# Kernel optimization log

Measured on AMD Instinct MI355X. Metric: run time of the kernel, lower is better.

Reference implementation:

```python
import jax, jax.numpy as jnp
import numpy as np

TOP_K = 2
CAPACITY_FACTOR = 1.0


def setup_inputs() -> dict:
    key = jax.random.key(0)
    ks = jax.random.split(key, 4)
    S, M, E, V = 32768, 512, 64, 2048
    return {
        "x": jax.random.normal(ks[0], (S, M), jnp.float32),
        "wg": jax.random.normal(ks[1], (E, M), jnp.float32) * (1.0 / np.sqrt(M)),
        "fc1_w": jax.random.normal(ks[2], (E, M, V), jnp.float32) * (1.0 / np.sqrt(M)),
        "fc1_b": jnp.zeros((E, V), jnp.float32),
        "fc2_w": jax.random.normal(ks[3], (E, V, M), jnp.float32) * (1.0 / np.sqrt(V)),
        "fc2_b": jnp.zeros((E, M), jnp.float32),
    }


def _moe_forward(x, wg, fc1_w, fc1_b, fc2_w, fc2_b):
    S, M = x.shape
    E = wg.shape[0]
    K = TOP_K
    # capacity = top_k * int(cap_factor * ceil(S / E))  (static, from shapes)
    C = K * int(CAPACITY_FACTOR * ((S + E - 1) // E))

    # --- gating ---
    logits = x @ wg.T                                    # [S, E]
    gates = jax.nn.softmax(logits, axis=-1)              # [S, E]
    topk_idx = jax.lax.top_k(logits, K)[1]               # [S, K] int32
    masks = jax.nn.one_hot(topk_idx, E, dtype=logits.dtype)  # [S, K, E]
    gates_s = jnp.einsum('se,ske->sk', gates, masks)     # [S, K]

    # load-balance aux loss (fp32 path of load_balance)
    me = gates.sum(axis=0)                               # [E]
    ce = masks[:, 0, :].sum(axis=0)                      # [E]
    l_loss = jnp.sum(me * ce) * (E / (S * S))

    # --- cumsum capacity locations with per-k offsets (acc_base) ---
    counts = masks.sum(axis=0)                           # [K, E]
    prev_counts = jnp.concatenate(
        [jnp.zeros((1, E), logits.dtype), jnp.cumsum(counts, axis=0)[:-1]], axis=0)
    cums = jnp.cumsum(masks, axis=0) - 1.0               # fast_cumsum_sub_one per k
    locs = jnp.einsum('ske,ske->sk', cums + prev_counts[None], masks).astype(jnp.int32)

    # normalize top-k gates (top_k > 1 branch)
    denom = jnp.maximum(gates_s.sum(axis=1, keepdims=True),
                        jnp.finfo(gates_s.dtype).eps)
    gates_n = gates_s / denom                            # [S, K]

    # --- encode: scatter tokens into [E, C, M], overflow tokens dropped ---
    valid = locs < C                                     # [S, K]
    flat_pos = jnp.where(valid, topk_idx.astype(jnp.int32) * C + locs, E * C)
    src = jnp.broadcast_to(x[:, None, :], (S, K, M)).reshape(-1, M)
    disp = jnp.zeros((E * C + 1, M), x.dtype).at[flat_pos.reshape(-1)].add(src)
    disp = disp[:E * C].reshape(E, C, M)                 # world_size=1: AllToAll = id

    # --- fused FFN experts: relu(x @ fc1 + b1) @ fc2 + b2 ---
    h = jax.nn.relu(jnp.einsum('ecm,emv->ecv', disp, fc1_w) + fc1_b[:, None, :])
    eout = jnp.einsum('ecv,evm->ecm', h, fc2_w) + fc2_b[:, None, :]

    # --- decode/combine: gather expert slots, weight by normalized gates ---
    eflat = jnp.concatenate([eout.reshape(E * C, M),
                             jnp.zeros((1, M), eout.dtype)], axis=0)
    gathered = eflat[flat_pos]                           # [S, K, M]
    y = jnp.einsum('sk,skm->sm', gates_n * valid.astype(gates_n.dtype), gathered)
    return y, l_loss


def reference(x, wg, fc1_w, fc1_b, fc2_w, fc2_b):
    return _moe_forward(x, wg, fc1_w, fc1_b, fc2_w, fc2_b)
```

## Files before the change

kernel.cpp:

```cpp
#include <hip/hip_runtime.h>
#include <hip/hip_bf16.h>
#include <stdint.h>

#define S_TOK 32768
#define M_DIM 512
#define E_NUM 64
#define V_DIM 2048
#define CAP   1024

typedef __attribute__((ext_vector_type(8))) short short8;
typedef __attribute__((ext_vector_type(4))) float f32x4;

__device__ __forceinline__ unsigned short f2bf(float f) {
  unsigned int u = __float_as_uint(f);
  unsigned int r = (u + 0x7fffu + ((u >> 16) & 1u)) >> 16;
  return (unsigned short)r;
}
__device__ __forceinline__ float bf2f(unsigned short h) {
  return __uint_as_float(((unsigned int)h) << 16);
}

__device__ __forceinline__ void gload16(const void* g, void* lds) {
  __builtin_amdgcn_global_load_lds(
      (const __attribute__((address_space(1))) void*)g,
      (__attribute__((address_space(3))) void*)lds, 16, 0, 0);
}

__global__ __launch_bounds__(256) void transpose_convert(const float* __restrict__ in,
                                                         unsigned short* __restrict__ out,
                                                         int R, int Cc) {
  __shared__ float tile[32][33];
  int b = blockIdx.z;
  const float* ip = in + (size_t)b * R * Cc;
  unsigned short* op = out + (size_t)b * R * Cc;
  int c0 = blockIdx.x * 32, r0 = blockIdx.y * 32;
  int tx = threadIdx.x & 31, ty = threadIdx.x >> 5;
  #pragma unroll
  for (int j = 0; j < 32; j += 8)
    tile[ty + j][tx] = ip[(size_t)(r0 + ty + j) * Cc + c0 + tx];
  __syncthreads();
  int tid = threadIdx.x;
  #pragma unroll
  for (int j = 0; j < 32; j += 16) {
    int c = (tid >> 4) + j;
    int r2 = (tid & 15) * 2;
    ushort2 o;
    o.x = f2bf(tile[r2][c]);
    o.y = f2bf(tile[r2 + 1][c]);
    *reinterpret_cast<ushort2*>(&op[(size_t)(c0 + c) * R + r0 + r2]) = o;
  }
}

__global__ __launch_bounds__(256) void gating_kernel(
    const float* __restrict__ x, const float* __restrict__ wg,
    int* __restrict__ topk, float* __restrict__ gates_n,
    float* __restrict__ me_part, int* __restrict__ ce_part,
    unsigned short* __restrict__ xbf) {
  __shared__ float4 xs4[16 * 128];
  __shared__ float mered[4][64];
  __shared__ int cered[4][64];
  int tid = threadIdx.x;
  int l = tid & 63, w = tid >> 6;
  int tb = blockIdx.x * 16;
  const float4* xg4 = reinterpret_cast<const float4*>(x) + (size_t)tb * 128;
  ushort4* xb4 = reinterpret_cast<ushort4*>(xbf) + (size_t)tb * 128;
  #pragma unroll
  for (int i = 0; i < 8; ++i) {
    float4 v = xg4[i * 256 + tid];
    xs4[i * 256 + tid] = v;
    ushort4 o;
    o.x = f2bf(v.x); o.y = f2bf(v.y); o.z = f2bf(v.z); o.w = f2bf(v.w);
    xb4[i * 256 + tid] = o;
  }
  __syncthreads();

  const float4* wg4 = reinterpret_cast<const float4*>(wg) + (size_t)l * 128;
  float acc[4] = {0.f, 0.f, 0.f, 0.f};
  for (int i = 0; i < 128; ++i) {
    float4 wv = wg4[i];
    #pragma unroll
    for (int t = 0; t < 4; ++t) {
      float4 xv = xs4[(w * 4 + t) * 128 + i];
      acc[t] += xv.x * wv.x; acc[t] += xv.y * wv.y;
      acc[t] += xv.z * wv.z; acc[t] += xv.w * wv.w;
    }
  }

  float melocal = 0.f;
  int celocal = 0;
  for (int t = 0; t < 4; ++t) {
    float v = acc[t];
    float bv = v; int bi = l;
    #pragma unroll
    for (int off = 32; off; off >>= 1) {
      float ov = __shfl_xor(bv, off);
      int oi = __shfl_xor(bi, off);
      if (ov > bv || (ov == bv && oi < bi)) { bv = ov; bi = oi; }
    }
    float v2 = (l == bi) ? -INFINITY : v;
    float bv2 = v2; int bi2 = l;
    #pragma unroll
    for (int off = 32; off; off >>= 1) {
      float ov = __shfl_xor(bv2, off);
      int oi = __shfl_xor(bi2, off);
      if (ov > bv2 || (ov == bv2 && oi < bi2)) { bv2 = ov; bi2 = oi; }
    }
    float ex = expf(v - bv);
    float s = ex;
    #pragma unroll
    for (int off = 32; off; off >>= 1) s += __shfl_xor(s, off);
    melocal += ex / s;
    if (l == bi) celocal += 1;
    if (l == 0) {
      int sidx = tb + w * 4 + t;
      topk[sidx * 2 + 0] = bi;
      topk[sidx * 2 + 1] = bi2;
      float g1 = 1.0f / s;
      float g2 = expf(bv2 - bv) / s;
      float denom = fmaxf(g1 + g2, 1.1920929e-07f);
      gates_n[sidx * 2 + 0] = g1 / denom;
      gates_n[sidx * 2 + 1] = g2 / denom;
    }
  }
  mered[w][l] = melocal;
  cered[w][l] = celocal;
  __syncthreads();
  if (tid < 64) {
    me_part[blockIdx.x * 64 + tid] =
        mered[0][tid] + mered[1][tid] + mered[2][tid] + mered[3][tid];
    ce_part[blockIdx.x * 64 + tid] =
        cered[0][tid] + cered[1][tid] + cered[2][tid] + cered[3][tid];
  }
}

__global__ __launch_bounds__(256) void rank_kernel(const int* __restrict__ topk,
                                                   int* __restrict__ dest,
                                                   int* __restrict__ slot_map) {
  int e = blockIdx.x;
  int tid = threadIdx.x;
  int l = tid & 63, w = tid >> 6;
  const int2* tk = reinterpret_cast<const int2*>(topk);
  int base = tid * 128;
  int c0 = 0, c1 = 0;
  for (int j = 0; j < 128; ++j) {
    int2 p = tk[base + j];
    c0 += (p.x == e); c1 += (p.y == e);
  }
  int i0 = c0, i1 = c1;
  #pragma unroll
  for (int off = 1; off < 64; off <<= 1) {
    int t0 = __shfl_up(i0, off);
    int t1 = __shfl_up(i1, off);
    if (l >= off) { i0 += t0; i1 += t1; }
  }
  __shared__ int ws0[4], ws1[4], wo0[4], wo1[4], tot0s;
  if (l == 63) { ws0[w] = i0; ws1[w] = i1; }
  __syncthreads();
  if (tid == 0) {
    int a = 0, b = 0;
    #pragma unroll
    for (int j = 0; j < 4; ++j) { wo0[j] = a; a += ws0[j]; wo1[j] = b; b += ws1[j]; }
    tot0s = a;
  }
  __syncthreads();
  int loc0 = wo0[w] + i0 - c0;
  int loc1 = tot0s + wo1[w] + i1 - c1;
  for (int j = 0; j < 128; ++j) {
    int s = base + j;
    int2 p = tk[s];
    if (p.x == e) {
      int d = (loc0 < CAP) ? e * CAP + loc0 : -1;
      dest[s * 2] = d;
      if (d >= 0) slot_map[d] = s;
      loc0++;
    }
    if (p.y == e) {
      int d = (loc1 < CAP) ? e * CAP + loc1 : -1;
      dest[s * 2 + 1] = d;
      if (d >= 0) slot_map[d] = s;
      loc1++;
    }
  }
}

#define PH_TOP                                                                 \
  __builtin_amdgcn_sched_barrier(0);                                           \
  __builtin_amdgcn_s_barrier();                                                \
  asm volatile("s_waitcnt lgkmcnt(0)" ::: "memory");                           \
  __builtin_amdgcn_sched_barrier(0);                                           \
  __builtin_amdgcn_s_setprio(1);
#define PH_BOT                                                                 \
  __builtin_amdgcn_s_setprio(0);                                               \
  __builtin_amdgcn_sched_barrier(0);                                           \
  __builtin_amdgcn_s_barrier();

struct SmemGemm {
  union {
    struct {
      unsigned short A[2][256 * 64];
      unsigned short B[2][256 * 64];
    } st;
    unsigned short C[256 * 258];
  };
};

template <int KD, int ND, int NBX, int NBY, bool GATHER, bool RELU>
__global__ __launch_bounds__(512, 2) void gemm8_kernel(
    const unsigned short* __restrict__ A,
    const unsigned short* __restrict__ BT,
    const float* __restrict__ bias,
    const int* __restrict__ slot_map,
    unsigned short* __restrict__ out) {
  constexpr int NT = KD / 64;
  __shared__ SmemGemm sm;

  const int tid = threadIdx.x;
  const int l = tid & 63;
  const int w = tid >> 6;
  const int wm = w >> 2;
  const int wn = w & 3;
  const int lr = l & 15;
  const int lk8 = l >> 4;

  const int nwg = E_NUM * NBX * NBY;
  const int cpx = nwg >> 3;
  int lid = ((int)blockIdx.x % 8) * cpx + (int)blockIdx.x / 8;
  const int e = lid / (NBX * NBY);
  int rem = lid % (NBX * NBY);
  const int n0 = (rem / NBY) * 256;
  const int r0 = (rem % NBY) * 256;

  const int cg8 = (((l & 7) ^ (l >> 3)) * 8);

  uint32_t offA[2][2], offB[2][2], ldsA[2][2], ldsB[2][2];
  #pragma unroll
  for (int sel = 0; sel < 2; ++sel) {
    #pragma unroll
    for (int i = 0; i < 2; ++i) {
      int lr128 = i * 64 + w * 8 + (l >> 3);
      int ar = ((lr128 >> 6) * 128) + sel * 64 + (lr128 & 63);
      int br = ((lr128 >> 5) * 64) + sel * 32 + (lr128 & 31);
      ldsA[sel][i] = ar * 64 + (l & 7) * 8;
      ldsB[sel][i] = br * 64 + (l & 7) * 8;
      int arow;
      if (GATHER) {
        int s = slot_map[e * CAP + r0 + ar];
        if (s < 0) s = 0;
        arow = s;
      } else {
        arow = e * CAP + r0 + ar;
      }
      offA[sel][i] = (uint32_t)arow * KD + cg8;
      offB[sel][i] = (uint32_t)(n0 + br) * KD + cg8;
    }
  }
  const unsigned short* Bexp = BT + (size_t)e * ND * KD;

#define STAGE_A(sel, p, kt)                                                    \
  do {                                                                         \
    gload16(A + offA[sel][0] + (kt) * 64, &sm.st.A[p][ldsA[sel][0]]);          \
    gload16(A + offA[sel][1] + (kt) * 64, &sm.st.A[p][ldsA[sel][1]]);          \
  } while (0)
#define STAGE_B(sel, p, kt)                                                    \
  do {                                                                         \
    gload16(Bexp + offB[sel][0] + (kt) * 64, &sm.st.B[p][ldsB[sel][0]]);       \
    gload16(Bexp + offB[sel][1] + (kt) * 64, &sm.st.B[p][ldsB[sel][1]]);       \
  } while (0)

  const int sg0 = ((0 + lk8) ^ (lr & 7)) * 8;
  const int sg1 = ((4 + lk8) ^ (lr & 7)) * 8;
#define RD_A(p, mh, mi, ks)                                                    \
  (*reinterpret_cast<const short8*>(                                           \
      &sm.st.A[p][(wm * 128 + (mh) * 64 + (mi) * 16 + lr) * 64 + ((ks) ? sg1 : sg0)]))
#define RD_B(p, nh, ni, ks)                                                    \
  (*reinterpret_cast<const short8*>(                                           \
      &sm.st.B[p][(wn * 64 + (nh) * 32 + (ni) * 16 + lr) * 64 + ((ks) ? sg1 : sg0)]))

  short8 afr[2][4][2];
  short8 bfr[2][2];
  f32x4 acc[8][4];
  f32x4 zero = {0.f, 0.f, 0.f, 0.f};
  #pragma unroll
  for (int m = 0; m < 8; ++m)
    #pragma unroll
    for (int n = 0; n < 4; ++n) acc[m][n] = zero;

  STAGE_A(0, 0, 0); STAGE_A(1, 0, 0); STAGE_B(0, 0, 0); STAGE_B(1, 0, 0);
  STAGE_A(0, 1, 1); STAGE_A(1, 1, 1); STAGE_B(0, 1, 1);
  asm volatile("s_waitcnt vmcnt(6)" ::: "memory");
  __builtin_amdgcn_sched_barrier(0);
  __builtin_amdgcn_s_barrier();

#define GROUP(k, p)                                                            \
  {                                                                            \
          \
    _Pragma("unroll") for (int mi = 0; mi < 4; ++mi) {                         \
      afr[0][mi][0] = RD_A(p, 0, mi, 0);                                       \
      afr[0][mi][1] = RD_A(p, 0, mi, 1);                                       \
    }                                                                          \
    _Pragma("unroll") for (int ni = 0; ni < 2; ++ni) {                         \
      bfr[ni][0] = RD_B(p, 0, ni, 0);                                          \
      bfr[ni][1] = RD_B(p, 0, ni, 1);                                          \
    }                                                                          \
    if ((k) + 1 < NT) { STAGE_B(1, (p) ^ 1, (k) + 1); }                        \
    PH_TOP                                                                     \
    _Pragma("unroll") for (int mi = 0; mi < 4; ++mi)                           \
      _Pragma("unroll") for (int ni = 0; ni < 2; ++ni) {                       \
        acc[mi][ni] = __builtin_amdgcn_mfma_f32_16x16x32_bf16(                 \
            afr[0][mi][0], bfr[ni][0], acc[mi][ni], 0, 0, 0);                  \
        acc[mi][ni] = __builtin_amdgcn_mfma_f32_16x16x32_bf16(                 \
            afr[0][mi][1], bfr[ni][1], acc[mi][ni], 0, 0, 0);                  \
      }                                                                        \
    PH_BOT                                                                     \
            \
    _Pragma("unroll") for (int mi = 0; mi < 4; ++mi) {                         \
      afr[1][mi][0] = RD_A(p, 1, mi, 0);                                       \
      afr[1][mi][1] = RD_A(p, 1, mi, 1);                                       \
    }                                                                          \
    if ((k) + 2 < NT) { STAGE_A(0, p, (k) + 2); }                              \
    PH_TOP                                                                     \
    _Pragma("unroll") for (int mi = 0; mi < 4; ++mi)                           \
      _Pragma("unroll") for (int ni = 0; ni < 2; ++ni) {                       \
        acc[4 + mi][ni] = __builtin_amdgcn_mfma_f32_16x16x32_bf16(             \
            afr[1][mi][0], bfr[ni][0], acc[4 + mi][ni], 0, 0, 0);              \
        acc[4 + mi][ni] = __builtin_amdgcn_mfma_f32_16x16x32_bf16(             \
            afr[1][mi][1], bfr[ni][1], acc[4 + mi][ni], 0, 0, 0);              \
      }                                                                        \
    PH_BOT                                                                     \
            \
    _Pragma("unroll") for (int ni = 0; ni < 2; ++ni) {                         \
      bfr[ni][0] = RD_B(p, 1, ni, 0);                                          \
      bfr[ni][1] = RD_B(p, 1, ni, 1);                                          \
    }                                                                          \
    if ((k) + 2 < NT) { STAGE_A(1, p, (k) + 2); }                              \
    PH_TOP                                                                     \
    _Pragma("unroll") for (int mi = 0; mi < 4; ++mi)                           \
      _Pragma("unroll") for (int ni = 0; ni < 2; ++ni) {                       \
        acc[mi][2 + ni] = __builtin_amdgcn_mfma_f32_16x16x32_bf16(             \
            afr[0][mi][0], bfr[ni][0], acc[mi][2 + ni], 0, 0, 0);              \
        acc[mi][2 + ni] = __builtin_amdgcn_mfma_f32_16x16x32_bf16(             \
            afr[0][mi][1], bfr[ni][1], acc[mi][2 + ni], 0, 0, 0);              \
      }                                                                        \
    PH_BOT                                                                     \
        \
    if ((k) + 2 < NT) { STAGE_B(0, p, (k) + 2); }                              \
    __builtin_amdgcn_sched_barrier(0);                                         \
    __builtin_amdgcn_s_barrier();                                              \
    __builtin_amdgcn_s_setprio(1);                                             \
    _Pragma("unroll") for (int mi = 0; mi < 4; ++mi)                           \
      _Pragma("unroll") for (int ni = 0; ni < 2; ++ni) {                       \
        acc[4 + mi][2 + ni] = __builtin_amdgcn_mfma_f32_16x16x32_bf16(         \
            afr[1][mi][0], bfr[ni][0], acc[4 + mi][2 + ni], 0, 0, 0);          \
        acc[4 + mi][2 + ni] = __builtin_amdgcn_mfma_f32_16x16x32_bf16(         \
            afr[1][mi][1], bfr[ni][1], acc[4 + mi][2 + ni], 0, 0, 0);          \
      }                                                                        \
    __builtin_amdgcn_s_setprio(0);                                             \
    __builtin_amdgcn_sched_barrier(0);                                         \
    if ((k) + 2 < NT) {                                                        \
      asm volatile("s_waitcnt vmcnt(6)" ::: "memory");                         \
    } else {                                                                   \
      asm volatile("s_waitcnt vmcnt(0)" ::: "memory");                         \
    }                                                                          \
    __builtin_amdgcn_sched_barrier(0);                                         \
    __builtin_amdgcn_s_barrier();                                              \
  }

  for (int kk = 0; kk < NT / 2; ++kk) {
    int k0 = 2 * kk;
    GROUP(k0, 0)
    GROUP(k0 + 1, 1)
  }
#undef GROUP
#undef STAGE_A
#undef STAGE_B
#undef RD_A
#undef RD_B

  #pragma unroll
  for (int n = 0; n < 4; ++n) {
    int gcl = wn * 64 + n * 16 + lr;
    float bv = bias[e * ND + n0 + gcl];
    #pragma unroll
    for (int m = 0; m < 8; ++m) {
      int trow = wm * 128 + m * 16 + lk8 * 4;
      #pragma unroll
      for (int j = 0; j < 4; ++j) {
        float v = acc[m][n][j] + bv;
        if (RELU) v = fmaxf(v, 0.f);
        sm.C[(trow + j) * 258 + gcl] = f2bf(v);
      }
    }
  }
  __syncthreads();
  #pragma unroll
  for (int i = 0; i < 16; ++i) {
    int chunk = i * 512 + tid;
    int row = chunk >> 5;
    int c8 = chunk & 31;
    short8 v = *reinterpret_cast<const short8*>(&sm.C[row * 258 + c8 * 8]);
    *reinterpret_cast<short8*>(
        &out[((size_t)(e * CAP + r0 + row)) * ND + n0 + c8 * 8]) = v;
  }
}

__global__ __launch_bounds__(256) void decode_kernel(
    const unsigned short* __restrict__ Y, const int* __restrict__ dest,
    const float* __restrict__ gn, float* __restrict__ y) {
  int t = blockIdx.x * 4 + (threadIdx.x >> 6);
  int m0 = (threadIdx.x & 63) * 8;
  int d0 = dest[t * 2 + 0], d1 = dest[t * 2 + 1];
  float g0 = gn[t * 2 + 0], g1 = gn[t * 2 + 1];
  float o[8];
  #pragma unroll
  for (int j = 0; j < 8; ++j) o[j] = 0.f;
  if (d0 >= 0) {
    short8 v = *reinterpret_cast<const short8*>(&Y[(size_t)d0 * M_DIM + m0]);
    #pragma unroll
    for (int j = 0; j < 8; ++j) o[j] += g0 * bf2f((unsigned short)v[j]);
  }
  if (d1 >= 0) {
    short8 v = *reinterpret_cast<const short8*>(&Y[(size_t)d1 * M_DIM + m0]);
    #pragma unroll
    for (int j = 0; j < 8; ++j) o[j] += g1 * bf2f((unsigned short)v[j]);
  }
  float4 o0 = {o[0], o[1], o[2], o[3]};
  float4 o1 = {o[4], o[5], o[6], o[7]};
  *reinterpret_cast<float4*>(&y[(size_t)t * M_DIM + m0]) = o0;
  *reinterpret_cast<float4*>(&y[(size_t)t * M_DIM + m0 + 4]) = o1;
}

__global__ __launch_bounds__(1024) void loss_kernel(const float* __restrict__ me_part,
                                                    const int* __restrict__ ce_part,
                                                    float* __restrict__ out) {
  int tid = threadIdx.x;
  int e = tid & 63, ch = tid >> 6;
  float sme = 0.f, sce = 0.f;
  for (int j = 0; j < 128; ++j) {
    int idx = (ch * 128 + j) * 64 + e;
    sme += me_part[idx];
    sce += (float)ce_part[idx];
  }
  __shared__ float redm[16][64];
  __shared__ float redc[16][64];
  redm[ch][e] = sme;
  redc[ch][e] = sce;
  __syncthreads();
  if (tid < 64) {
    float m = 0.f, c = 0.f;
    #pragma unroll
    for (int k = 0; k < 16; ++k) { m += redm[k][tid]; c += redc[k][tid]; }
    float p = m * c;
    #pragma unroll
    for (int off = 32; off; off >>= 1) p += __shfl_xor(p, off);
    if (tid == 0) out[0] = p * ((float)E_NUM / ((float)S_TOK * (float)S_TOK));
  }
}

extern "C" void kernel_launch(void* const* d_in, const int* in_sizes, int n_in,
                              void* d_out, int out_size, void* d_ws, size_t ws_size,
                              hipStream_t stream) {
  const float* x     = (const float*)d_in[0];
  const float* wg    = (const float*)d_in[1];
  const float* fc1_w = (const float*)d_in[2];
  const float* fc1_b = (const float*)d_in[3];
  const float* fc2_w = (const float*)d_in[4];
  const float* fc2_b = (const float*)d_in[5];
  float* y = (float*)d_out;
  float* loss_out = y + (size_t)S_TOK * M_DIM;

  char* ws = (char*)d_ws;
  size_t off = 0;
  auto alloc = [&](size_t bytes) {
    char* p = ws + off;
    off += (bytes + 255) & ~(size_t)255;
    return p;
  };
  unsigned short* wT1 = (unsigned short*)alloc((size_t)E_NUM * V_DIM * M_DIM * 2);
  unsigned short* wT2 = (unsigned short*)alloc((size_t)E_NUM * M_DIM * V_DIM * 2);
  unsigned short* H   = (unsigned short*)alloc((size_t)E_NUM * CAP * V_DIM * 2);
  unsigned short* xbf = (unsigned short*)alloc((size_t)S_TOK * M_DIM * 2);
  int*   topk     = (int*)alloc((size_t)S_TOK * 2 * 4);
  float* gatesn   = (float*)alloc((size_t)S_TOK * 2 * 4);
  int*   dest     = (int*)alloc((size_t)S_TOK * 2 * 4);
  int*   slot_map = (int*)alloc((size_t)E_NUM * CAP * 4);
  float* me_part  = (float*)alloc((size_t)(S_TOK / 16) * 64 * 4);
  int*   ce_part  = (int*)alloc((size_t)(S_TOK / 16) * 64 * 4);
  unsigned short* Y = wT1;

  (void)hipMemsetAsync(slot_map, 0xFF, (size_t)E_NUM * CAP * 4, stream);

  transpose_convert<<<dim3(V_DIM / 32, M_DIM / 32, E_NUM), 256, 0, stream>>>(fc1_w, wT1, M_DIM, V_DIM);
  transpose_convert<<<dim3(M_DIM / 32, V_DIM / 32, E_NUM), 256, 0, stream>>>(fc2_w, wT2, V_DIM, M_DIM);

  gating_kernel<<<S_TOK / 16, 256, 0, stream>>>(x, wg, topk, gatesn, me_part, ce_part, xbf);
  rank_kernel<<<E_NUM, 256, 0, stream>>>(topk, dest, slot_map);

  gemm8_kernel<512, 2048, 8, 4, true, true>
      <<<E_NUM * 8 * 4, 512, 0, stream>>>(xbf, wT1, fc1_b, slot_map, H);
  gemm8_kernel<2048, 512, 2, 4, false, false>
      <<<E_NUM * 2 * 4, 512, 0, stream>>>(H, wT2, fc2_b, slot_map, Y);

  decode_kernel<<<S_TOK / 4, 256, 0, stream>>>(Y, dest, gatesn, y);
  loss_kernel<<<1, 1024, 0, stream>>>(me_part, ce_part, loss_out);
}
```

Baseline: 775.8 us.

## Loop fc1 GEMM over row tiles per block and widen transpose tiles

The fc1 expert GEMM now launches one block per (expert, N-tile) that loops over all four 256-row tiles, instead of one block per output tile. Each block reuses its B column tile across the loop (likely via cache), which shrinks the grid from 2048 to 512 blocks. That reduces parallelism and serialises the epilogue with the next tile's prologue. Separately, the weight transpose/convert kernel moves to 64x64 tiles with float4 loads and 16-byte bf16 stores, to get wider memory transactions.

```diff
diff --git a/kernel.cpp b/kernel.cpp
--- a/kernel.cpp
+++ b/kernel.cpp
@@ -29,25 +29,31 @@
 __global__ __launch_bounds__(256) void transpose_convert(const float* __restrict__ in,
                                                          unsigned short* __restrict__ out,
                                                          int R, int Cc) {
-  __shared__ float tile[32][33];
+  __shared__ float ts[64][65];
   int b = blockIdx.z;
   const float* ip = in + (size_t)b * R * Cc;
   unsigned short* op = out + (size_t)b * R * Cc;
-  int c0 = blockIdx.x * 32, r0 = blockIdx.y * 32;
-  int tx = threadIdx.x & 31, ty = threadIdx.x >> 5;
+  int c0 = blockIdx.x * 64, r0 = blockIdx.y * 64;
+  int tid = threadIdx.x;
+  int lrow = tid >> 4;
+  int lc4 = (tid & 15) * 4;
   #pragma unroll
-  for (int j = 0; j < 32; j += 8)
-    tile[ty + j][tx] = ip[(size_t)(r0 + ty + j) * Cc + c0 + tx];
+  for (int i = 0; i < 4; ++i) {
+    int row = i * 16 + lrow;
+    float4 v = *reinterpret_cast<const float4*>(&ip[(size_t)(r0 + row) * Cc + c0 + lc4]);
+    ts[row][lc4 + 0] = v.x; ts[row][lc4 + 1] = v.y;
+    ts[row][lc4 + 2] = v.z; ts[row][lc4 + 3] = v.w;
+  }
   __syncthreads();
-  int tid = threadIdx.x;
   #pragma unroll
-  for (int j = 0; j < 32; j += 16) {
-    int c = (tid >> 4) + j;
-    int r2 = (tid & 15) * 2;
-    ushort2 o;
-    o.x = f2bf(tile[r2][c]);
-    o.y = f2bf(tile[r2 + 1][c]);
-    *reinterpret_cast<ushort2*>(&op[(size_t)(c0 + c) * R + r0 + r2]) = o;
+  for (int i = 0; i < 2; ++i) {
+    int chunk = i * 256 + tid;
+    int c = chunk >> 3;
+    int rg = (chunk & 7) * 8;
+    short8 o;
+    #pragma unroll
+    for (int j = 0; j < 8; ++j) o[j] = (short)f2bf(ts[rg + j][c]);
+    *reinterpret_cast<short8*>(&op[(size_t)(c0 + c) * R + r0 + rg]) = o;
   }
 }
 
@@ -204,7 +210,7 @@
   };
 };
 
-template <int KD, int ND, int NBX, int NBY, bool GATHER, bool RELU>
+template <int KD, int ND, int NBX, int NBY, int NLOOP, bool GATHER, bool RELU>
 __global__ __launch_bounds__(512, 2) void gemm8_kernel(
     const unsigned short* __restrict__ A,
     const unsigned short* __restrict__ BT,
@@ -212,6 +218,7 @@
     const int* __restrict__ slot_map,
     unsigned short* __restrict__ out) {
   constexpr int NT = KD / 64;
+  constexpr int NBYG = NBY / NLOOP;
   __shared__ SmemGemm sm;
 
   const int tid = threadIdx.x;
@@ -222,17 +229,18 @@
   const int lr = l & 15;
   const int lk8 = l >> 4;
 
-  const int nwg = E_NUM * NBX * NBY;
+  const int nwg = E_NUM * NBX * NBYG;
   const int cpx = nwg >> 3;
   int lid = ((int)blockIdx.x % 8) * cpx + (int)blockIdx.x / 8;
-  const int e = lid / (NBX * NBY);
-  int rem = lid % (NBX * NBY);
-  const int n0 = (rem / NBY) * 256;
-  const int r0 = (rem % NBY) * 256;
+  const int e = lid / (NBX * NBYG);
+  int rem = lid % (NBX * NBYG);
+  const int n0 = (rem / NBYG) * 256;
+  const int r0base = (rem % NBYG) * (NLOOP * 256);
 
   const int cg8 = (((l & 7) ^ (l >> 3)) * 8);
 
-  uint32_t offA[2][2], offB[2][2], ldsA[2][2], ldsB[2][2];
+  int arows[2][2];
+  uint32_t offB[2][2], ldsA[2][2], ldsB[2][2];
   #pragma unroll
   for (int sel = 0; sel < 2; ++sel) {
     #pragma unroll
@@ -240,21 +248,16 @@
       int lr128 = i * 64 + w * 8 + (l >> 3);
       int ar = ((lr128 >> 6) * 128) + sel * 64 + (lr128 & 63);
       int br = ((lr128 >> 5) * 64) + sel * 32 + (lr128 & 31);
+      arows[sel][i] = ar;
       ldsA[sel][i] = ar * 64 + (l & 7) * 8;
       ldsB[sel][i] = br * 64 + (l & 7) * 8;
-      int arow;
-      if (GATHER) {
-        int s = slot_map[e * CAP + r0 + ar];
-        if (s < 0) s = 0;
-        arow = s;
-      } else {
-        arow = e * CAP + r0 + ar;
-      }
-      offA[sel][i] = (uint32_t)arow * KD + cg8;
       offB[sel][i] = (uint32_t)(n0 + br) * KD + cg8;
     }
   }
   const unsigned short* Bexp = BT + (size_t)e * ND * KD;
+
+  const int sg0 = ((0 + lk8) ^ (lr & 7)) * 8;
+  const int sg1 = ((4 + lk8) ^ (lr & 7)) * 8;
 
 #define STAGE_A(sel, p, kt)                                                    \
   do {                                                                         \
@@ -266,9 +269,6 @@
     gload16(Bexp + offB[sel][0] + (kt) * 64, &sm.st.B[p][ldsB[sel][0]]);       \
     gload16(Bexp + offB[sel][1] + (kt) * 64, &sm.st.B[p][ldsB[sel][1]]);       \
   } while (0)
-
-  const int sg0 = ((0 + lk8) ^ (lr & 7)) * 8;
-  const int sg1 = ((4 + lk8) ^ (lr & 7)) * 8;
 #define RD_A(p, mh, mi, ks)                                                    \
   (*reinterpret_cast<const short8*>(                                           \
       &sm.st.A[p][(wm * 128 + (mh) * 64 + (mi) * 16 + lr) * 64 + ((ks) ? sg1 : sg0)]))
@@ -280,20 +280,40 @@
   short8 bfr[2][2];
   f32x4 acc[8][4];
   f32x4 zero = {0.f, 0.f, 0.f, 0.f};
-  #pragma unroll
-  for (int m = 0; m < 8; ++m)
-    #pragma unroll
-    for (int n = 0; n < 4; ++n) acc[m][n] = zero;
-
-  STAGE_A(0, 0, 0); STAGE_A(1, 0, 0); STAGE_B(0, 0, 0); STAGE_B(1, 0, 0);
-  STAGE_A(0, 1, 1); STAGE_A(1, 1, 1); STAGE_B(0, 1, 1);
-  asm volatile("s_waitcnt vmcnt(6)" ::: "memory");
-  __builtin_amdgcn_sched_barrier(0);
-  __builtin_amdgcn_s_barrier();
+
+  for (int it = 0; it < NLOOP; ++it) {
+    const int r0 = r0base + it * 256;
+    uint32_t offA[2][2];
+    #pragma unroll
+    for (int sel = 0; sel < 2; ++sel) {
+      #pragma unroll
+      for (int i = 0; i < 2; ++i) {
+        int ar = arows[sel][i];
+        int arow;
+        if (GATHER) {
+          int s = slot_map[e * CAP + r0 + ar];
+          if (s < 0) s = 0;
+          arow = s;
+        } else {
+          arow = e * CAP + r0 + ar;
+        }
+        offA[sel][i] = (uint32_t)arow * KD + cg8;
+      }
+    }
+    #pragma unroll
+    for (int m = 0; m < 8; ++m)
+      #pragma unroll
+      for (int n = 0; n < 4; ++n) acc[m][n] = zero;
+
+    STAGE_A(0, 0, 0); STAGE_A(1, 0, 0); STAGE_B(0, 0, 0); STAGE_B(1, 0, 0);
+    STAGE_A(0, 1, 1); STAGE_A(1, 1, 1); STAGE_B(0, 1, 1);
+    asm volatile("s_waitcnt vmcnt(6)" ::: "memory");
+    __builtin_amdgcn_sched_barrier(0);
+    __builtin_amdgcn_s_barrier();
 
 #define GROUP(k, p)                                                            \
   {                                                                            \
-          \
+               \
     _Pragma("unroll") for (int mi = 0; mi < 4; ++mi) {                         \
       afr[0][mi][0] = RD_A(p, 0, mi, 0);                                       \
       afr[0][mi][1] = RD_A(p, 0, mi, 1);                                       \
@@ -312,7 +332,7 @@
             afr[0][mi][1], bfr[ni][1], acc[mi][ni], 0, 0, 0);                  \
       }                                                                        \
     PH_BOT                                                                     \
-            \
+                 \
     _Pragma("unroll") for (int mi = 0; mi < 4; ++mi) {                         \
       afr[1][mi][0] = RD_A(p, 1, mi, 0);                                       \
       afr[1][mi][1] = RD_A(p, 1, mi, 1);                                       \
@@ -327,7 +347,7 @@
             afr[1][mi][1], bfr[ni][1], acc[4 + mi][ni], 0, 0, 0);              \
       }                                                                        \
     PH_BOT                                                                     \
-            \
+                 \
     _Pragma("unroll") for (int ni = 0; ni < 2; ++ni) {                         \
       bfr[ni][0] = RD_B(p, 1, ni, 0);                                          \
       bfr[ni][1] = RD_B(p, 1, ni, 1);                                          \
@@ -342,7 +362,7 @@
             afr[0][mi][1], bfr[ni][1], acc[mi][2 + ni], 0, 0, 0);              \
       }                                                                        \
     PH_BOT                                                                     \
-        \
+             \
     if ((k) + 2 < NT) { STAGE_B(0, p, (k) + 2); }                              \
     __builtin_amdgcn_sched_barrier(0);                                         \
     __builtin_amdgcn_s_barrier();                                              \
@@ -365,42 +385,45 @@
     __builtin_amdgcn_s_barrier();                                              \
   }
 
-  for (int kk = 0; kk < NT / 2; ++kk) {
-    int k0 = 2 * kk;
-    GROUP(k0, 0)
-    GROUP(k0 + 1, 1)
-  }
+    for (int kk = 0; kk < NT / 2; ++kk) {
+      int k0 = 2 * kk;
+      GROUP(k0, 0)
+      GROUP(k0 + 1, 1)
+    }
 #undef GROUP
+
+    #pragma unroll
+    for (int n = 0; n < 4; ++n) {
+      int gcl = wn * 64 + n * 16 + lr;
+      float bv = bias[e * ND + n0 + gcl];
+      #pragma unroll
+      for (int m = 0; m < 8; ++m) {
+        int trow = wm * 128 + m * 16 + lk8 * 4;
+        #pragma unroll
+        for (int j = 0; j < 4; ++j) {
+          float v = acc[m][n][j] + bv;
+          if (RELU) v = fmaxf(v, 0.f);
+          sm.C[(trow + j) * 258 + gcl] = f2bf(v);
+        }
+      }
+    }
+    __syncthreads();
+    #pragma unroll
+    for (int i = 0; i < 16; ++i) {
+      int chunk = i * 512 + tid;
+      int row = chunk >> 5;
+      int c8 = chunk & 31;
+      short8 v = *reinterpret_cast<const short8*>(&sm.C[row * 258 + c8 * 8]);
+      *reinterpret_cast<short8*>(
+          &out[((size_t)(e * CAP + r0 + row)) * ND + n0 + c8 * 8]) = v;
+    }
+    asm volatile("s_waitcnt vmcnt(0)" ::: "memory");
+    __syncthreads();
+  }
 #undef STAGE_A
 #undef STAGE_B
 #undef RD_A
 #undef RD_B
-
-  #pragma unroll
-  for (int n = 0; n < 4; ++n) {
-    int gcl = wn * 64 + n * 16 + lr;
-    float bv = bias[e * ND + n0 + gcl];
-    #pragma unroll
-    for (int m = 0; m < 8; ++m) {
-      int trow = wm * 128 + m * 16 + lk8 * 4;
-      #pragma unroll
-      for (int j = 0; j < 4; ++j) {
-        float v = acc[m][n][j] + bv;
-        if (RELU) v = fmaxf(v, 0.f);
-        sm.C[(trow + j) * 258 + gcl] = f2bf(v);
-      }
-    }
-  }
-  __syncthreads();
-  #pragma unroll
-  for (int i = 0; i < 16; ++i) {
-    int chunk = i * 512 + tid;
-    int row = chunk >> 5;
-    int c8 = chunk & 31;
-    short8 v = *reinterpret_cast<const short8*>(&sm.C[row * 258 + c8 * 8]);
-    *reinterpret_cast<short8*>(
-        &out[((size_t)(e * CAP + r0 + row)) * ND + n0 + c8 * 8]) = v;
-  }
 }
 
 __global__ __launch_bounds__(256) void decode_kernel(
@@ -489,15 +512,15 @@
 
   (void)hipMemsetAsync(slot_map, 0xFF, (size_t)E_NUM * CAP * 4, stream);
 
-  transpose_convert<<<dim3(V_DIM / 32, M_DIM / 32, E_NUM), 256, 0, stream>>>(fc1_w, wT1, M_DIM, V_DIM);
-  transpose_convert<<<dim3(M_DIM / 32, V_DIM / 32, E_NUM), 256, 0, stream>>>(fc2_w, wT2, V_DIM, M_DIM);
+  transpose_convert<<<dim3(V_DIM / 64, M_DIM / 64, E_NUM), 256, 0, stream>>>(fc1_w, wT1, M_DIM, V_DIM);
+  transpose_convert<<<dim3(M_DIM / 64, V_DIM / 64, E_NUM), 256, 0, stream>>>(fc2_w, wT2, V_DIM, M_DIM);
 
   gating_kernel<<<S_TOK / 16, 256, 0, stream>>>(x, wg, topk, gatesn, me_part, ce_part, xbf);
   rank_kernel<<<E_NUM, 256, 0, stream>>>(topk, dest, slot_map);
 
-  gemm8_kernel<512, 2048, 8, 4, true, true>
-      <<<E_NUM * 8 * 4, 512, 0, stream>>>(xbf, wT1, fc1_b, slot_map, H);
-  gemm8_kernel<2048, 512, 2, 4, false, false>
+  gemm8_kernel<512, 2048, 8, 4, 4, true, true>
+      <<<E_NUM * 8, 512, 0, stream>>>(xbf, wT1, fc1_b, slot_map, H);
+  gemm8_kernel<2048, 512, 2, 4, 1, false, false>
       <<<E_NUM * 2 * 4, 512, 0, stream>>>(H, wT2, fc2_b, slot_map, Y);
 
   decode_kernel<<<S_TOK / 4, 256, 0, stream>>>(Y, dest, gatesn, y);
```

Result: slower. 830.5 us (+7.0%).
